# Kernel optimization log

Hardware: AMD Instinct MI355X
Metric: run time of the kernel (lower is better)

## Reference

```python
import jax, jax.numpy as jnp
import numpy as np

N = 50000      # nodes
E = 800000     # edges (before self loops)
G = 256        # graphs in batch
N_IN, NHID, HEADS, NOUT = 128, 64, 2, 768
ATT_SLOPE = 0.2   # GATv2 attention LeakyReLU slope (PyG default)
ACT_SLOPE = 0.01  # nn.LeakyReLU default slope


def setup_inputs() -> dict:
    key = jax.random.key(0)
    ks = jax.random.split(key, 20)
    def lin_w(k, fo, fi):
        return (jax.random.normal(k, (fo, fi), jnp.float32) / np.sqrt(fi)).astype(jnp.float32)
    x = jax.random.normal(ks[0], (N, N_IN), jnp.float32)
    edge_index = jax.random.randint(ks[1], (2, E), 0, N, dtype=jnp.int64)
    batch = jnp.sort(jax.random.randint(ks[2], (N,), 0, G, dtype=jnp.int64))
    HC = HEADS * NHID
    return {
        "x": x, "edge_index": edge_index, "batch": batch,
        # conv1: GATv2Conv(N_IN -> NHID, heads=HEADS)
        "w1_l": lin_w(ks[3], HC, N_IN), "b1_l": jnp.zeros((HC,), jnp.float32),
        "w1_r": lin_w(ks[4], HC, N_IN), "b1_r": jnp.zeros((HC,), jnp.float32),
        "att1": jax.random.normal(ks[5], (HEADS, NHID), jnp.float32) / np.sqrt(NHID),
        "bias1": jnp.zeros((HC,), jnp.float32),
        # conv2: GATv2Conv(HC -> NHID, heads=1)
        "w2_l": lin_w(ks[6], NHID, HC), "b2_l": jnp.zeros((NHID,), jnp.float32),
        "w2_r": lin_w(ks[7], NHID, HC), "b2_r": jnp.zeros((NHID,), jnp.float32),
        "att2": jax.random.normal(ks[8], (1, NHID), jnp.float32) / np.sqrt(NHID),
        "bias2": jnp.zeros((NHID,), jnp.float32),
        # MLP head
        "fc1_w": lin_w(ks[9], NHID, NHID), "fc1_b": jnp.zeros((NHID,), jnp.float32),
        "fc2_w": lin_w(ks[10], NOUT, NHID), "fc2_b": jnp.zeros((NOUT,), jnp.float32),
    }


def _leaky(v, slope):
    return jnp.where(v > 0, v, slope * v)


def gatv2_conv(x, src, dst, w_l, b_l, w_r, b_r, att, bias, heads, ch):
    n = x.shape[0]
    xl = (x @ w_l.T + b_l).reshape(n, heads, ch)   # source transform
    xr = (x @ w_r.T + b_r).reshape(n, heads, ch)   # target transform
    m = _leaky(xl[src] + xr[dst], ATT_SLOPE)       # [E, H, C]
    e = jnp.einsum('ehc,hc->eh', m, att)           # attention logits
    # segment softmax over incoming edges of each dst node (self loops guarantee non-empty)
    emax = jax.ops.segment_max(e, dst, num_segments=n)
    ex = jnp.exp(e - emax[dst])
    denom = jax.ops.segment_sum(ex, dst, num_segments=n)
    alpha = ex / denom[dst]
    out = jax.ops.segment_sum(xl[src] * alpha[:, :, None], dst, num_segments=n)
    return out.reshape(n, heads * ch) + bias


def reference(x, edge_index, batch, w1_l, b1_l, w1_r, b1_r, att1, bias1,
              w2_l, b2_l, w2_r, b2_r, att2, bias2, fc1_w, fc1_b, fc2_w, fc2_b):
    loops = jnp.arange(N, dtype=edge_index.dtype)
    src = jnp.concatenate([edge_index[0], loops])  # PyG adds self loops by default
    dst = jnp.concatenate([edge_index[1], loops])
    h = gatv2_conv(x, src, dst, w1_l, b1_l, w1_r, b1_r, att1, bias1, HEADS, NHID)
    h = _leaky(h, ACT_SLOPE)
    h = gatv2_conv(h, src, dst, w2_l, b2_l, w2_r, b2_r, att2, bias2, 1, NHID)
    h = _leaky(h, ACT_SLOPE)
    # global mean pool over graphs
    sums = jax.ops.segment_sum(h, batch, num_segments=G)
    cnt = jax.ops.segment_sum(jnp.ones((N,), h.dtype), batch, num_segments=G)
    pooled = sums / jnp.maximum(cnt, 1.0)[:, None]
    h = _leaky(pooled @ fc1_w.T + fc1_b, ACT_SLOPE)
    return h @ fc2_w.T + fc2_b
```

## Files before the change

### kernel.cpp

```cpp
#include <hip/hip_runtime.h>

#define ATT_SLOPE 0.2f
#define ACT_SLOPE 0.01f

typedef _Float16 half8  __attribute__((ext_vector_type(8)));
typedef _Float16 half2v __attribute__((ext_vector_type(2)));
typedef float    floatx4 __attribute__((ext_vector_type(4)));

#if defined(__has_builtin)
#if __has_builtin(__builtin_amdgcn_fdot2)
#define HAVE_FDOT2 1
#endif
#endif

__device__ __forceinline__ float lrelu(float v, float s) {
    return fmaxf(v, v * s);
}

__device__ __forceinline__ half2v lrelu2(half2v m) {
    half2v t = m * (_Float16)ATT_SLOPE;
    return __builtin_elementwise_max(m, t);
}

__device__ __forceinline__ float dot2(half2v a, half2v b, float c) {
#ifdef HAVE_FDOT2
    return __builtin_amdgcn_fdot2(a, b, c, false);
#else
    return c + (float)a[0] * (float)b[0] + (float)a[1] * (float)b[1];
#endif
}


__global__ __launch_bounds__(256) void k_count(const int* __restrict__ ei, int E, int N,
                                               int* __restrict__ deg) {
    int i = blockIdx.x * 256 + threadIdx.x;
    int total = E + N;
    if (i >= total) return;
    int dst = (i < E) ? ei[E + i] : (i - E);
    atomicAdd(&deg[dst], 1);
}

__global__ __launch_bounds__(256) void k_scan_block(const int* __restrict__ deg, int n,
                                                    int* __restrict__ rp1, int* __restrict__ bsum) {
    __shared__ int s[256];
    int tid = threadIdx.x;
    int i = blockIdx.x * 256 + tid;
    s[tid] = (i < n) ? deg[i] : 0;
    __syncthreads();
    for (int off = 1; off < 256; off <<= 1) {
        int t = (tid >= off) ? s[tid - off] : 0;
        __syncthreads();
        s[tid] += t;
        __syncthreads();
    }
    if (i < n) rp1[i] = s[tid];
    if (tid == 255) bsum[blockIdx.x] = s[255];
}

__global__ __launch_bounds__(256) void k_scan_bsum(const int* __restrict__ bsum, int nb,
                                                   int* __restrict__ boff) {
    __shared__ int s[256];
    int tid = threadIdx.x;
    s[tid] = (tid < nb) ? bsum[tid] : 0;
    __syncthreads();
    for (int off = 1; off < 256; off <<= 1) {
        int t = (tid >= off) ? s[tid - off] : 0;
        __syncthreads();
        s[tid] += t;
        __syncthreads();
    }
    if (tid < nb) boff[tid] = (tid > 0) ? s[tid - 1] : 0;
}

__global__ __launch_bounds__(256) void k_scan_add(int* __restrict__ rowptr,
                                                  const int* __restrict__ boff, int n) {
    int i = blockIdx.x * 256 + threadIdx.x;
    if (i < n) rowptr[i + 1] += boff[blockIdx.x];
    if (i == 0) rowptr[0] = 0;
}

__global__ __launch_bounds__(256) void k_scatter(const int* __restrict__ ei, int E, int N,
                                                 const int* __restrict__ rowptr,
                                                 int* __restrict__ cursor,
                                                 int* __restrict__ adj) {
    int i = blockIdx.x * 256 + threadIdx.x;
    int total = E + N;
    if (i >= total) return;
    int src, dst;
    if (i < E) { src = ei[i]; dst = ei[E + i]; } else { src = i - E; dst = i - E; }
    int pos = atomicAdd(&cursor[dst], 1);
    adj[rowptr[dst] + pos] = src;
}


__global__ __launch_bounds__(256) void k_encode_w(const float* __restrict__ w1l,
                                                  const float* __restrict__ w1r,
                                                  const float* __restrict__ w2l,
                                                  const float* __restrict__ w2r,
                                                  _Float16* __restrict__ W1h,
                                                  _Float16* __restrict__ W1lo,
                                                  _Float16* __restrict__ W2h,
                                                  _Float16* __restrict__ W2lo) {
    int i = blockIdx.x * 256 + threadIdx.x;
    if (i >= 49152) return;
    float v;
    _Float16 *ph, *pl;
    int idx;
    if (i < 32768) {
        idx = i;
        v = (i < 16384) ? w1l[i] : w1r[i - 16384];
        ph = W1h; pl = W1lo;
    } else {
        int j = i - 32768;
        idx = j;
        v = (j < 8192) ? w2l[j] : w2r[j - 8192];
        ph = W2h; pl = W2lo;
    }
    _Float16 h = (_Float16)v;
    ph[idx] = h;
    pl[idx] = (_Float16)(v - (float)h);
}


template <int COUT, bool IN_F32>
__global__ __launch_bounds__(512) void gemm_mfma(const float* __restrict__ Af,
                                                 const _Float16* __restrict__ Ahi,
                                                 const _Float16* __restrict__ Alo, int n_rows,
                                                 const _Float16* __restrict__ Whi,
                                                 const _Float16* __restrict__ Wlo,
                                                 const float* __restrict__ B0,
                                                 const float* __restrict__ B1,
                                                 _Float16* __restrict__ out) {
    constexpr int NT = COUT / 16;
    constexpr int WS = 40;
    __shared__ _Float16 sWh[COUT][WS];
    __shared__ _Float16 sWl[COUT][WS];
    const int tid = threadIdx.x;
    const int lane = tid & 63, wv = tid >> 6;
    const int m = lane & 15, q = lane >> 4;
    const long row0 = ((long)blockIdx.x * 8 + wv) * 16;
    const bool active = row0 < n_rows;
    const long arow = row0 + m;

    floatx4 acc[NT] = {};
    for (int kk = 0; kk < 128; kk += 32) {
        __syncthreads();
        for (int t = tid; t < COUT * 4; t += 512) {
            int c = t >> 2, ch = t & 3;
            *(half8*)&sWh[c][ch * 8] = *(const half8*)&Whi[(size_t)c * 128 + kk + ch * 8];
            *(half8*)&sWl[c][ch * 8] = *(const half8*)&Wlo[(size_t)c * 128 + kk + ch * 8];
        }
        __syncthreads();
        if (active) {
            half8 ah, al;
            if constexpr (IN_F32) {
                float4 a0 = *(const float4*)&Af[(size_t)arow * 128 + kk + q * 8];
                float4 a1 = *(const float4*)&Af[(size_t)arow * 128 + kk + q * 8 + 4];
                float av[8] = {a0.x, a0.y, a0.z, a0.w, a1.x, a1.y, a1.z, a1.w};
                #pragma unroll
                for (int x = 0; x < 8; ++x) {
                    ah[x] = (_Float16)av[x];
                    al[x] = (_Float16)(av[x] - (float)ah[x]);
                }
            } else {
                ah = *(const half8*)&Ahi[(size_t)arow * 128 + kk + q * 8];
                al = *(const half8*)&Alo[(size_t)arow * 128 + kk + q * 8];
            }
            #pragma unroll
            for (int nt = 0; nt < NT; ++nt) {
                half8 bh = *(const half8*)&sWh[nt * 16 + m][q * 8];
                half8 bl = *(const half8*)&sWl[nt * 16 + m][q * 8];
                acc[nt] = __builtin_amdgcn_mfma_f32_16x16x32_f16(ah, bh, acc[nt], 0, 0, 0);
                acc[nt] = __builtin_amdgcn_mfma_f32_16x16x32_f16(al, bh, acc[nt], 0, 0, 0);
                acc[nt] = __builtin_amdgcn_mfma_f32_16x16x32_f16(ah, bl, acc[nt], 0, 0, 0);
            }
        }
    }
    if (active) {
        #pragma unroll
        for (int nt = 0; nt < NT; ++nt) {
            int col = nt * 16 + m;
            float b = (col < COUT / 2) ? B0[col] : B1[col - COUT / 2];
            #pragma unroll
            for (int r = 0; r < 4; ++r) {
                long grow = row0 + q * 4 + r;
                out[(size_t)grow * COUT + col] = (_Float16)(acc[nt][r] + b);
            }
        }
    }
}


__global__ __launch_bounds__(256) void conv1_fused(const _Float16* __restrict__ buf,
                                                   const int* __restrict__ rowptr,
                                                   const int* __restrict__ adj,
                                                   const float* __restrict__ att,
                                                   const float* __restrict__ bias,
                                                   _Float16* __restrict__ h1hi,
                                                   _Float16* __restrict__ h1lo, int n) {
    __shared__ _Float16 sxl[4][32][136];
    __shared__ _Float16 sxr[4][128];
    __shared__ float    sw[4][2][32];
    __shared__ _Float16 satt[128];
    const int tid = threadIdx.x, lane = tid & 63, wv = tid >> 6;
    if (tid < 128) satt[tid] = (_Float16)att[tid];
    __syncthreads();
    int node = blockIdx.x * 4 + wv;
    if (node >= n) return;

    const int jlane = lane & 31;
    const int grp = lane >> 5;
    const int chbase = grp * 64;
    if (lane < 16)
        *(half8*)&sxr[wv][lane * 8] = *(const half8*)&buf[(size_t)node * 256 + 128 + lane * 8];
    asm volatile("s_waitcnt lgkmcnt(0)" ::: "memory");

    const int s = rowptr[node], e = rowptr[node + 1];
    float2 acc = {0.f, 0.f};
    float den = 0.f;
    for (int c0 = s; c0 < e; c0 += 32) {
        const int cnt = min(32, e - c0);
        if (jlane < cnt) {
            int src = adj[c0 + jlane];
            const _Float16* xlp = &buf[(size_t)src * 256 + chbase];
            float sacc = 0.f;
            #pragma unroll
            for (int k = 0; k < 8; ++k) {
                half8 l = *(const half8*)&xlp[k * 8];
                half8 r = *(const half8*)&sxr[wv][chbase + k * 8];
                half8 a = *(const half8*)&satt[chbase + k * 8];
                *(half8*)&sxl[wv][jlane][chbase + k * 8] = l;
                #pragma unroll
                for (int p = 0; p < 4; ++p) {
                    half2v lp = {l[2 * p], l[2 * p + 1]};
                    half2v rp = {r[2 * p], r[2 * p + 1]};
                    half2v ap = {a[2 * p], a[2 * p + 1]};
                    sacc = dot2(lrelu2(lp + rp), ap, sacc);
                }
                #pragma unroll
                for (int p = 4; p < 8; ++p) {
                    half2v lp = {l[2 * p], l[2 * p + 1]};
                    half2v rp = {r[2 * p], r[2 * p + 1]};
                    half2v ap = {a[2 * p], a[2 * p + 1]};
                    sacc = dot2(lrelu2(lp + rp), ap, sacc);
                }
            }
            sw[wv][grp][jlane] = __expf(sacc);
        }
        asm volatile("s_waitcnt lgkmcnt(0)" ::: "memory");
        for (int j = 0; j < cnt; ++j) {
            float w = sw[wv][grp][j];
            half2v v = *(const half2v*)&sxl[wv][j][lane * 2];
            acc.x += w * (float)v[0];
            acc.y += w * (float)v[1];
            den += w;
        }
        asm volatile("s_waitcnt lgkmcnt(0)" ::: "memory");
    }
    float inv = 1.f / den;
    float2 b = *(const float2*)&bias[lane * 2];
    float ox = lrelu(acc.x * inv + b.x, ACT_SLOPE);
    float oy = lrelu(acc.y * inv + b.y, ACT_SLOPE);
    half2v hv, lv;
    hv[0] = (_Float16)ox; lv[0] = (_Float16)(ox - (float)hv[0]);
    hv[1] = (_Float16)oy; lv[1] = (_Float16)(oy - (float)hv[1]);
    *(half2v*)&h1hi[(size_t)node * 128 + lane * 2] = hv;
    *(half2v*)&h1lo[(size_t)node * 128 + lane * 2] = lv;
}


__global__ __launch_bounds__(256) void conv2_fused(const _Float16* __restrict__ buf,
                                                   const int* __restrict__ rowptr,
                                                   const int* __restrict__ adj,
                                                   const float* __restrict__ att,
                                                   const float* __restrict__ bias,
                                                   float* __restrict__ h2, int n) {
    __shared__ _Float16 sxl[4][32][72];
    __shared__ _Float16 sxr[4][64];
    __shared__ float    sw[4][32];
    __shared__ _Float16 satt[64];
    const int tid = threadIdx.x, lane = tid & 63, wv = tid >> 6;
    if (tid < 64) satt[tid] = (_Float16)att[tid];
    __syncthreads();
    int node = blockIdx.x * 4 + wv;
    if (node >= n) return;

    const int jlane = lane & 31;
    const int grp = lane >> 5;
    const int chbase = grp * 32;
    if (lane < 8)
        *(half8*)&sxr[wv][lane * 8] = *(const half8*)&buf[(size_t)node * 128 + 64 + lane * 8];
    asm volatile("s_waitcnt lgkmcnt(0)" ::: "memory");

    const int s = rowptr[node], e = rowptr[node + 1];
    float acc = 0.f, den = 0.f;
    for (int c0 = s; c0 < e; c0 += 32) {
        const int cnt = min(32, e - c0);
        float sacc = 0.f;
        if (jlane < cnt) {
            int src = adj[c0 + jlane];
            const _Float16* xlp = &buf[(size_t)src * 128 + chbase];
            #pragma unroll
            for (int k = 0; k < 4; ++k) {
                half8 l = *(const half8*)&xlp[k * 8];
                half8 r = *(const half8*)&sxr[wv][chbase + k * 8];
                half8 a = *(const half8*)&satt[chbase + k * 8];
                *(half8*)&sxl[wv][jlane][chbase + k * 8] = l;
                #pragma unroll
                for (int p = 0; p < 4; ++p) {
                    half2v lp = {l[2 * p], l[2 * p + 1]};
                    half2v rp = {r[2 * p], r[2 * p + 1]};
                    half2v ap = {a[2 * p], a[2 * p + 1]};
                    sacc = dot2(lrelu2(lp + rp), ap, sacc);
                }
            }
        }
        float efull = sacc + __shfl_xor(sacc, 32);
        if (grp == 0 && jlane < cnt) sw[wv][jlane] = __expf(efull);
        asm volatile("s_waitcnt lgkmcnt(0)" ::: "memory");
        for (int j = 0; j < cnt; ++j) {
            float w = sw[wv][j];
            acc += w * (float)sxl[wv][j][lane];
            den += w;
        }
        asm volatile("s_waitcnt lgkmcnt(0)" ::: "memory");
    }
    h2[(size_t)node * 64 + lane] = lrelu(acc / den + bias[lane], ACT_SLOPE);
}


__device__ __forceinline__ int lower_bound(const int* a, int n, int v) {
    int lo = 0, hi = n;
    while (lo < hi) { int mid = (lo + hi) >> 1; if (a[mid] < v) lo = mid + 1; else hi = mid; }
    return lo;
}

__global__ __launch_bounds__(256) void pool_mlp(const float* __restrict__ h2,
                                                const int* __restrict__ batch,
                                                const float* __restrict__ fc1_w,
                                                const float* __restrict__ fc1_b,
                                                const float* __restrict__ fc2_w,
                                                const float* __restrict__ fc2_b,
                                                float* __restrict__ out, int n) {
    const int g = blockIdx.x;
    const int tid = threadIdx.x;
    const int c = tid & 63, q = tid >> 6;
    __shared__ float partial[4][64];
    __shared__ float pooled[64];
    __shared__ float hmid[64];

    int lo = lower_bound(batch, n, g);
    int hi = lower_bound(batch, n, g + 1);

    float sum = 0.f;
    for (int i = lo + q; i < hi; i += 4) sum += h2[(size_t)i * 64 + c];
    partial[q][c] = sum;
    __syncthreads();
    if (q == 0) {
        float s = partial[0][c] + partial[1][c] + partial[2][c] + partial[3][c];
        int cnt = hi - lo;
        pooled[c] = s / (float)max(cnt, 1);
    }
    __syncthreads();
    if (tid < 64) {
        float acc = fc1_b[tid];
        const float* w = &fc1_w[(size_t)tid * 64];
        #pragma unroll
        for (int k = 0; k < 64; ++k) acc += pooled[k] * w[k];
        hmid[tid] = lrelu(acc, ACT_SLOPE);
    }
    __syncthreads();
    for (int o = tid; o < 768; o += 256) {
        float acc = fc2_b[o];
        const float* w = &fc2_w[(size_t)o * 64];
        #pragma unroll
        for (int k = 0; k < 64; ++k) acc += hmid[k] * w[k];
        out[(size_t)g * 768 + o] = acc;
    }
}


extern "C" void kernel_launch(void* const* d_in, const int* in_sizes, int n_in,
                              void* d_out, int out_size, void* d_ws, size_t ws_size,
                              hipStream_t stream) {
    const float* x     = (const float*)d_in[0];
    const int*   ei    = (const int*)d_in[1];
    const int*   batch = (const int*)d_in[2];
    const float* w1_l  = (const float*)d_in[3];
    const float* b1_l  = (const float*)d_in[4];
    const float* w1_r  = (const float*)d_in[5];
    const float* b1_r  = (const float*)d_in[6];
    const float* att1  = (const float*)d_in[7];
    const float* bias1 = (const float*)d_in[8];
    const float* w2_l  = (const float*)d_in[9];
    const float* b2_l  = (const float*)d_in[10];
    const float* w2_r  = (const float*)d_in[11];
    const float* b2_r  = (const float*)d_in[12];
    const float* att2  = (const float*)d_in[13];
    const float* bias2 = (const float*)d_in[14];
    const float* fc1_w = (const float*)d_in[15];
    const float* fc1_b = (const float*)d_in[16];
    const float* fc2_w = (const float*)d_in[17];
    const float* fc2_b = (const float*)d_in[18];
    float* out = (float*)d_out;

    const int N = in_sizes[2];
    const int E = in_sizes[1] / 2;
    const int T = E + N;
    const int G = out_size / 768;

    char* ws = (char*)d_ws;
    size_t off = 0;
    auto alloc = [&](size_t bytes) -> void* {
        void* p = ws + off;
        off = (off + bytes + 255) & ~(size_t)255;
        return p;
    };
    int*      deg    = (int*)alloc((size_t)N * 4);
    int*      rowptr = (int*)alloc((size_t)(N + 1) * 4);
    int*      cursor = (int*)alloc((size_t)N * 4);
    int*      bsum   = (int*)alloc(1024);
    int*      boff   = (int*)alloc(1024);
    int*      adj    = (int*)alloc((size_t)T * 4);
    _Float16* h1hi   = (_Float16*)alloc((size_t)N * 128 * 2);
    _Float16* h1lo   = (_Float16*)alloc((size_t)N * 128 * 2);
    _Float16* W1h    = (_Float16*)alloc(32768 * 2);
    _Float16* W1lo   = (_Float16*)alloc(32768 * 2);
    _Float16* W2h    = (_Float16*)alloc(16384 * 2);
    _Float16* W2lo   = (_Float16*)alloc(16384 * 2);
    _Float16* buf1   = (_Float16*)alloc((size_t)N * 256 * 2);
    _Float16* buf2 = buf1;
    float*    h2   = (float*)((char*)buf1 + (size_t)N * 256);

    const int nbN  = (N + 255) / 256;
    const int nbT  = (T + 255) / 256;
    const int mfmG = (N / 16 + 7) / 8;
    const int edgG = (N + 3) / 4;

    hipMemsetAsync(deg, 0, (size_t)N * 4, stream);
    k_count<<<nbT, 256, 0, stream>>>(ei, E, N, deg);
    k_scan_block<<<nbN, 256, 0, stream>>>(deg, N, rowptr + 1, bsum);
    k_scan_bsum<<<1, 256, 0, stream>>>(bsum, nbN, boff);
    k_scan_add<<<nbN, 256, 0, stream>>>(rowptr, boff, N);
    hipMemsetAsync(cursor, 0, (size_t)N * 4, stream);
    k_scatter<<<nbT, 256, 0, stream>>>(ei, E, N, rowptr, cursor, adj);

    k_encode_w<<<192, 256, 0, stream>>>(w1_l, w1_r, w2_l, w2_r, W1h, W1lo, W2h, W2lo);

    gemm_mfma<256, true><<<mfmG, 512, 0, stream>>>(x, nullptr, nullptr, N,
                                                   W1h, W1lo, b1_l, b1_r, buf1);
    conv1_fused<<<edgG, 256, 0, stream>>>(buf1, rowptr, adj, att1, bias1, h1hi, h1lo, N);

    gemm_mfma<128, false><<<mfmG, 512, 0, stream>>>(nullptr, h1hi, h1lo, N,
                                                    W2h, W2lo, b2_l, b2_r, buf2);
    conv2_fused<<<edgG, 256, 0, stream>>>(buf2, rowptr, adj, att2, bias2, h2, N);

    pool_mlp<<<G, 256, 0, stream>>>(h2, batch, fc1_w, fc1_b, fc2_w, fc2_b, out, N);
}
```

Measured before the change: 353.5 us.

## Split edge chunks to 16 per wave with 4 lane groups per channel slice

Both GATv2 aggregation kernels now process 16 edges per chunk instead of 32. Each edge's channels are split across four lane groups, and the partial logits are combined with extra cross-lane shuffles. The weighted-sum loop is unrolled by two with dual accumulators to break the dependency chain. With an average in-degree of about 17 (16 edges plus the self loop), this targets idle lanes in the 32-wide gather and shortens the per-lane serial dot product. The cost is extra shuffles and more loop iterations for high-degree nodes.

New measurement: 339.0 us. 1.04x faster.

```diff
diff --git a/kernel.cpp b/kernel.cpp
--- a/kernel.cpp
+++ b/kernel.cpp
@@ -198,9 +198,9 @@
                                                    const float* __restrict__ bias,
                                                    _Float16* __restrict__ h1hi,
                                                    _Float16* __restrict__ h1lo, int n) {
-    __shared__ _Float16 sxl[4][32][136];
+    __shared__ _Float16 sxl[4][16][136];
     __shared__ _Float16 sxr[4][128];
-    __shared__ float    sw[4][2][32];
+    __shared__ float    sw[4][2][16];
     __shared__ _Float16 satt[128];
     const int tid = threadIdx.x, lane = tid & 63, wv = tid >> 6;
     if (tid < 128) satt[tid] = (_Float16)att[tid];
@@ -208,59 +208,63 @@
     int node = blockIdx.x * 4 + wv;
     if (node >= n) return;
 
-    const int jlane = lane & 31;
-    const int grp = lane >> 5;
-    const int chbase = grp * 64;
+    const int jlane = lane & 15;
+    const int grp = lane >> 4;
+    const int chq = grp * 32;
+    const int head = grp >> 1;
+    const int wselg = lane >> 5;
     if (lane < 16)
         *(half8*)&sxr[wv][lane * 8] = *(const half8*)&buf[(size_t)node * 256 + 128 + lane * 8];
     asm volatile("s_waitcnt lgkmcnt(0)" ::: "memory");
 
     const int s = rowptr[node], e = rowptr[node + 1];
-    float2 acc = {0.f, 0.f};
-    float den = 0.f;
-    for (int c0 = s; c0 < e; c0 += 32) {
-        const int cnt = min(32, e - c0);
+    float2 accA = {0.f, 0.f}, accB = {0.f, 0.f};
+    float denA = 0.f, denB = 0.f;
+    for (int c0 = s; c0 < e; c0 += 16) {
+        const int cnt = min(16, e - c0);
+        float sacc0 = 0.f, sacc1 = 0.f;
         if (jlane < cnt) {
             int src = adj[c0 + jlane];
-            const _Float16* xlp = &buf[(size_t)src * 256 + chbase];
-            float sacc = 0.f;
+            const _Float16* xlp = &buf[(size_t)src * 256 + chq];
             #pragma unroll
-            for (int k = 0; k < 8; ++k) {
+            for (int k = 0; k < 4; ++k) {
                 half8 l = *(const half8*)&xlp[k * 8];
-                half8 r = *(const half8*)&sxr[wv][chbase + k * 8];
-                half8 a = *(const half8*)&satt[chbase + k * 8];
-                *(half8*)&sxl[wv][jlane][chbase + k * 8] = l;
+                half8 r = *(const half8*)&sxr[wv][chq + k * 8];
+                half8 a = *(const half8*)&satt[chq + k * 8];
+                *(half8*)&sxl[wv][jlane][chq + k * 8] = l;
+                float* sp = (k & 1) ? &sacc1 : &sacc0;
                 #pragma unroll
                 for (int p = 0; p < 4; ++p) {
                     half2v lp = {l[2 * p], l[2 * p + 1]};
                     half2v rp = {r[2 * p], r[2 * p + 1]};
                     half2v ap = {a[2 * p], a[2 * p + 1]};
-                    sacc = dot2(lrelu2(lp + rp), ap, sacc);
-                }
-                #pragma unroll
-                for (int p = 4; p < 8; ++p) {
-                    half2v lp = {l[2 * p], l[2 * p + 1]};
-                    half2v rp = {r[2 * p], r[2 * p + 1]};
-                    half2v ap = {a[2 * p], a[2 * p + 1]};
-                    sacc = dot2(lrelu2(lp + rp), ap, sacc);
+                    *sp = dot2(lrelu2(lp + rp), ap, *sp);
                 }
             }
-            sw[wv][grp][jlane] = __expf(sacc);
-        }
+        }
+        float sacc = sacc0 + sacc1;
+        float efull = sacc + __shfl_xor(sacc, 16);
+        if ((grp & 1) == 0 && jlane < cnt) sw[wv][head][jlane] = __expf(efull);
         asm volatile("s_waitcnt lgkmcnt(0)" ::: "memory");
-        for (int j = 0; j < cnt; ++j) {
-            float w = sw[wv][grp][j];
-            half2v v = *(const half2v*)&sxl[wv][j][lane * 2];
-            acc.x += w * (float)v[0];
-            acc.y += w * (float)v[1];
-            den += w;
+        int j = 0;
+        for (; j + 1 < cnt; j += 2) {
+            float w0 = sw[wv][wselg][j], w1 = sw[wv][wselg][j + 1];
+            half2v v0 = *(const half2v*)&sxl[wv][j][lane * 2];
+            half2v v1 = *(const half2v*)&sxl[wv][j + 1][lane * 2];
+            accA.x += w0 * (float)v0[0]; accA.y += w0 * (float)v0[1]; denA += w0;
+            accB.x += w1 * (float)v1[0]; accB.y += w1 * (float)v1[1]; denB += w1;
+        }
+        if (j < cnt) {
+            float w0 = sw[wv][wselg][j];
+            half2v v0 = *(const half2v*)&sxl[wv][j][lane * 2];
+            accA.x += w0 * (float)v0[0]; accA.y += w0 * (float)v0[1]; denA += w0;
         }
         asm volatile("s_waitcnt lgkmcnt(0)" ::: "memory");
     }
-    float inv = 1.f / den;
+    float inv = 1.f / (denA + denB);
     float2 b = *(const float2*)&bias[lane * 2];
-    float ox = lrelu(acc.x * inv + b.x, ACT_SLOPE);
-    float oy = lrelu(acc.y * inv + b.y, ACT_SLOPE);
+    float ox = lrelu((accA.x + accB.x) * inv + b.x, ACT_SLOPE);
+    float oy = lrelu((accA.y + accB.y) * inv + b.y, ACT_SLOPE);
     half2v hv, lv;
     hv[0] = (_Float16)ox; lv[0] = (_Float16)(ox - (float)hv[0]);
     hv[1] = (_Float16)oy; lv[1] = (_Float16)(oy - (float)hv[1]);
@@ -275,9 +279,9 @@
                                                    const float* __restrict__ att,
                                                    const float* __restrict__ bias,
                                                    float* __restrict__ h2, int n) {
-    __shared__ _Float16 sxl[4][32][72];
+    __shared__ _Float16 sxl[4][16][72];
     __shared__ _Float16 sxr[4][64];
-    __shared__ float    sw[4][32];
+    __shared__ float    sw[4][16];
     __shared__ _Float16 satt[64];
     const int tid = threadIdx.x, lane = tid & 63, wv = tid >> 6;
     if (tid < 64) satt[tid] = (_Float16)att[tid];
@@ -285,27 +289,27 @@
     int node = blockIdx.x * 4 + wv;
     if (node >= n) return;
 
-    const int jlane = lane & 31;
-    const int grp = lane >> 5;
-    const int chbase = grp * 32;
+    const int jlane = lane & 15;
+    const int grp = lane >> 4;
+    const int chq = grp * 16;
     if (lane < 8)
         *(half8*)&sxr[wv][lane * 8] = *(const half8*)&buf[(size_t)node * 128 + 64 + lane * 8];
     asm volatile("s_waitcnt lgkmcnt(0)" ::: "memory");
 
     const int s = rowptr[node], e = rowptr[node + 1];
-    float acc = 0.f, den = 0.f;
-    for (int c0 = s; c0 < e; c0 += 32) {
-        const int cnt = min(32, e - c0);
+    float accA = 0.f, accB = 0.f, denA = 0.f, denB = 0.f;
+    for (int c0 = s; c0 < e; c0 += 16) {
+        const int cnt = min(16, e - c0);
         float sacc = 0.f;
         if (jlane < cnt) {
             int src = adj[c0 + jlane];
-            const _Float16* xlp = &buf[(size_t)src * 128 + chbase];
+            const _Float16* xlp = &buf[(size_t)src * 128 + chq];
             #pragma unroll
-            for (int k = 0; k < 4; ++k) {
+            for (int k = 0; k < 2; ++k) {
                 half8 l = *(const half8*)&xlp[k * 8];
-                half8 r = *(const half8*)&sxr[wv][chbase + k * 8];
-                half8 a = *(const half8*)&satt[chbase + k * 8];
-                *(half8*)&sxl[wv][jlane][chbase + k * 8] = l;
+                half8 r = *(const half8*)&sxr[wv][chq + k * 8];
+                half8 a = *(const half8*)&satt[chq + k * 8];
+                *(half8*)&sxl[wv][jlane][chq + k * 8] = l;
                 #pragma unroll
                 for (int p = 0; p < 4; ++p) {
                     half2v lp = {l[2 * p], l[2 * p + 1]};
@@ -315,17 +319,24 @@
                 }
             }
         }
-        float efull = sacc + __shfl_xor(sacc, 32);
+        float s1 = sacc + __shfl_xor(sacc, 16);
+        float efull = s1 + __shfl_xor(s1, 32);
         if (grp == 0 && jlane < cnt) sw[wv][jlane] = __expf(efull);
         asm volatile("s_waitcnt lgkmcnt(0)" ::: "memory");
-        for (int j = 0; j < cnt; ++j) {
-            float w = sw[wv][j];
-            acc += w * (float)sxl[wv][j][lane];
-            den += w;
+        int j = 0;
+        for (; j + 1 < cnt; j += 2) {
+            float w0 = sw[wv][j], w1 = sw[wv][j + 1];
+            accA += w0 * (float)sxl[wv][j][lane];     denA += w0;
+            accB += w1 * (float)sxl[wv][j + 1][lane]; denB += w1;
+        }
+        if (j < cnt) {
+            float w0 = sw[wv][j];
+            accA += w0 * (float)sxl[wv][j][lane];
+            denA += w0;
         }
         asm volatile("s_waitcnt lgkmcnt(0)" ::: "memory");
     }
-    h2[(size_t)node * 64 + lane] = lrelu(acc / den + bias[lane], ACT_SLOPE);
+    h2[(size_t)node * 64 + lane] = lrelu((accA + accB) / (denA + denB) + bias[lane], ACT_SLOPE);
 }
 
 
```
